# Kernel optimization log

Hardware: AMD Instinct MI355X
Metric: run time of the kernel (lower is better)

The kernel has to match this reference:

```python
import jax, jax.numpy as jnp
import numpy as np

B, C, H, W = 16, 64, 64, 64
HEADS = 8

def conv1x1(x, w):
    # x: [B, Cin, H, W], w: [Cout, Cin] -> [B, Cout, H, W]
    return jnp.einsum('oc,bchw->bohw', w, x)

def maxpool2x2(x):
    b, c, h, w = x.shape
    return x.reshape(b, c, h // 2, 2, w // 2, 2).max(axis=(3, 5))

def setup_inputs() -> dict:
    key = jax.random.key(0)
    ks = jax.random.split(key, 6)
    x = jax.random.normal(ks[0], (B, C, H, W), dtype=jnp.float32)
    w_theta = jax.random.normal(ks[1], (C // HEADS, C), dtype=jnp.float32) * 0.05
    w_phi = jax.random.normal(ks[2], (C // HEADS, C), dtype=jnp.float32) * 0.05
    w_g = jax.random.normal(ks[3], (C // 2, C), dtype=jnp.float32) * 0.05
    w_o = jax.random.normal(ks[4], (C, C // 2), dtype=jnp.float32) * 0.05
    gamma = jax.random.normal(ks[5], (), dtype=jnp.float32)
    return {'x': x, 'w_theta': w_theta, 'w_phi': w_phi, 'w_g': w_g, 'w_o': w_o, 'gamma': gamma}

def reference(x, w_theta, w_phi, w_g, w_o, gamma):
    b, c, h, w = x.shape
    n = h * w                      # query length
    m = n // 4                     # kv length after 2x2 maxpool
    theta = conv1x1(x, w_theta).reshape(b, c // HEADS, n)   # [B, C/h, N]
    phi = maxpool2x2(conv1x1(x, w_phi)).reshape(b, c // HEADS, m)  # [B, C/h, M]
    g = maxpool2x2(conv1x1(x, w_g)).reshape(b, c // 2, m)   # [B, C/2, M]
    # attention: theta^T @ phi -> [B, N, M]; NOTE: no 1/sqrt(d) scaling (SAGAN)
    beta = jax.nn.softmax(jnp.einsum('bdn,bdm->bnm', theta, phi), axis=-1)
    # o = g @ beta^T -> [B, C/2, N]
    o = jnp.einsum('bdm,bnm->bdn', g, beta).reshape(b, c // 2, h, w)
    o = conv1x1(o, w_o)            # [B, C, H, W]
    return gamma * o + x
```

## Files before the change

kernel.cpp:

```cpp
#include <hip/hip_runtime.h>
#include <hip/hip_bf16.h>

#define NB 16
#define NC 64
#define NN 4096
#define NM 1024
#define ND 8
#define NG 32

typedef short short8 __attribute__((ext_vector_type(8)));
typedef float floatx4 __attribute__((ext_vector_type(4)));

#define LOG2E 1.44269504f

__device__ __forceinline__ short f2bfs(float f) {
    union { __hip_bfloat16 h; short s; } u;
    u.h = __float2bfloat16(f);
    return u.s;
}
__device__ __forceinline__ unsigned pack2bf(float a, float b) {
    return (unsigned)(unsigned short)f2bfs(a) | ((unsigned)(unsigned short)f2bfs(b) << 16);
}
__device__ __forceinline__ unsigned pk2fast(float a, float b) {
    unsigned ua = __float_as_uint(a) + 0x8000u;
    unsigned ub = __float_as_uint(b) + 0x8000u;
    return __builtin_amdgcn_perm(ub, ua, 0x07060302);
}
__device__ __forceinline__ short8 u4s8(uint4 v) {
    union { uint4 u; short8 s; } c; c.u = v; return c.s;
}

__global__ __launch_bounds__(256)
void proj_kernel(const float* __restrict__ x,
                 const float* __restrict__ w_theta,
                 const float* __restrict__ w_phi,
                 const float* __restrict__ w_g,
                 const float* __restrict__ w_o,
                 unsigned* __restrict__ theta_ws,
                 unsigned* __restrict__ phi_ws,
                 unsigned* __restrict__ g2_ws)
{
    __shared__ __align__(16) float xl[64 * 128];
    __shared__ float lwt[512];
    __shared__ float lwp[512];
    __shared__ __align__(8) float lwgT[64 * 34];
    __shared__ float lwoT[32 * 65];
    __shared__ __align__(16) float lgs[32 * 36];
    __shared__ float lps[32 * 8];

    const int b  = blockIdx.x >> 5;
    const int ph = blockIdx.x & 31;
    const int t  = threadIdx.x;

    for (int i = t; i < 512;  i += 256) { lwt[i] = w_theta[i]; lwp[i] = w_phi[i]; }
    for (int i = t; i < 2048; i += 256) {
        lwgT[(i & 63) * 34 + (i >> 6)] = w_g[i];
        lwoT[(i & 31) * 65 + (i >> 5)] = w_o[i];
    }

    const float* xb = x + (size_t)b * NC * NN + (size_t)ph * 128;
    for (int idx = t; idx < 2048; idx += 256) {
        int c = idx >> 5, i4 = idx & 31;
        ((float4*)xl)[c * 32 + i4] = ((const float4*)(xb + (size_t)c * NN))[i4];
    }
    __syncthreads();

    if (t < 128) {
        float th[8];
        #pragma unroll
        for (int oc = 0; oc < 8; ++oc) th[oc] = 0.f;
        for (int c = 0; c < 64; ++c) {
            float xv = xl[c * 128 + t];
            #pragma unroll
            for (int oc = 0; oc < 8; ++oc) th[oc] = fmaf(lwt[oc * 64 + c], xv, th[oc]);
        }
        uint4 pk;
        pk.x = pack2bf(th[0] * LOG2E, th[1] * LOG2E);
        pk.y = pack2bf(th[2] * LOG2E, th[3] * LOG2E);
        pk.z = pack2bf(th[4] * LOG2E, th[5] * LOG2E);
        pk.w = pack2bf(th[6] * LOG2E, th[7] * LOG2E);
        ((uint4*)theta_ws)[(size_t)b * NN + ph * 128 + t] = pk;

        int m = t >> 2, oc0 = (t & 3) * 2;
        float s[2][4];
        #pragma unroll
        for (int a = 0; a < 2; ++a)
            #pragma unroll
            for (int p = 0; p < 4; ++p) s[a][p] = 0.f;
        #pragma unroll 4
        for (int c = 0; c < 64; ++c) {
            const float* xr = &xl[c * 128];
            float x0 = xr[2 * m], x1 = xr[2 * m + 1], x2 = xr[64 + 2 * m], x3 = xr[65 + 2 * m];
            #pragma unroll
            for (int a = 0; a < 2; ++a) {
                float w = lwp[(oc0 + a) * 64 + c];
                s[a][0] = fmaf(w, x0, s[a][0]);
                s[a][1] = fmaf(w, x1, s[a][1]);
                s[a][2] = fmaf(w, x2, s[a][2]);
                s[a][3] = fmaf(w, x3, s[a][3]);
            }
        }
        #pragma unroll
        for (int a = 0; a < 2; ++a)
            lps[m * 8 + oc0 + a] = fmaxf(fmaxf(s[a][0], s[a][1]), fmaxf(s[a][2], s[a][3]));
    } else {
        int tt = t - 128;
        int oc0 = (tt >> 3) * 2, grp = tt & 7;
        float s0[16], s1[16];
        #pragma unroll
        for (int i = 0; i < 16; ++i) { s0[i] = 0.f; s1[i] = 0.f; }
        const float4* xl4 = (const float4*)xl;
        #pragma unroll 2
        for (int c = 0; c < 64; ++c) {
            float4 a0 = xl4[c * 32 + 2 * grp];
            float4 a1 = xl4[c * 32 + 2 * grp + 1];
            float4 b0 = xl4[c * 32 + 16 + 2 * grp];
            float4 b1 = xl4[c * 32 + 17 + 2 * grp];
            float2 wv = *(const float2*)&lwgT[c * 34 + oc0];
            float w0 = wv.x, w1 = wv.y;
            s0[0] = fmaf(w0, a0.x, s0[0]);  s0[1] = fmaf(w0, a0.y, s0[1]);
            s0[2] = fmaf(w0, a0.z, s0[2]);  s0[3] = fmaf(w0, a0.w, s0[3]);
            s0[4] = fmaf(w0, a1.x, s0[4]);  s0[5] = fmaf(w0, a1.y, s0[5]);
            s0[6] = fmaf(w0, a1.z, s0[6]);  s0[7] = fmaf(w0, a1.w, s0[7]);
            s0[8] = fmaf(w0, b0.x, s0[8]);  s0[9] = fmaf(w0, b0.y, s0[9]);
            s0[10] = fmaf(w0, b0.z, s0[10]); s0[11] = fmaf(w0, b0.w, s0[11]);
            s0[12] = fmaf(w0, b1.x, s0[12]); s0[13] = fmaf(w0, b1.y, s0[13]);
            s0[14] = fmaf(w0, b1.z, s0[14]); s0[15] = fmaf(w0, b1.w, s0[15]);
            s1[0] = fmaf(w1, a0.x, s1[0]);  s1[1] = fmaf(w1, a0.y, s1[1]);
            s1[2] = fmaf(w1, a0.z, s1[2]);  s1[3] = fmaf(w1, a0.w, s1[3]);
            s1[4] = fmaf(w1, a1.x, s1[4]);  s1[5] = fmaf(w1, a1.y, s1[5]);
            s1[6] = fmaf(w1, a1.z, s1[6]);  s1[7] = fmaf(w1, a1.w, s1[7]);
            s1[8] = fmaf(w1, b0.x, s1[8]);  s1[9] = fmaf(w1, b0.y, s1[9]);
            s1[10] = fmaf(w1, b0.z, s1[10]); s1[11] = fmaf(w1, b0.w, s1[11]);
            s1[12] = fmaf(w1, b1.x, s1[12]); s1[13] = fmaf(w1, b1.y, s1[13]);
            s1[14] = fmaf(w1, b1.z, s1[14]); s1[15] = fmaf(w1, b1.w, s1[15]);
        }
        #pragma unroll
        for (int p = 0; p < 4; ++p) {
            float v0 = fmaxf(fmaxf(s0[2 * p], s0[2 * p + 1]), fmaxf(s0[8 + 2 * p], s0[9 + 2 * p]));
            float v1 = fmaxf(fmaxf(s1[2 * p], s1[2 * p + 1]), fmaxf(s1[8 + 2 * p], s1[9 + 2 * p]));
            lgs[oc0 * 36 + grp * 4 + p]       = v0;
            lgs[(oc0 + 1) * 36 + grp * 4 + p] = v1;
        }
    }
    __syncthreads();

    {
        int co = t >> 2, sel = t & 3;
        int m0a = 4 * sel, m0b = 16 + 4 * sel;
        float v[8];
        #pragma unroll
        for (int mm = 0; mm < 8; ++mm) v[mm] = 0.f;
        #pragma unroll 4
        for (int c = 0; c < 32; ++c) {
            float w = lwoT[c * 65 + co];
            float4 ga = *(const float4*)&lgs[c * 36 + m0a];
            float4 gb = *(const float4*)&lgs[c * 36 + m0b];
            v[0] = fmaf(w, ga.x, v[0]); v[1] = fmaf(w, ga.y, v[1]);
            v[2] = fmaf(w, ga.z, v[2]); v[3] = fmaf(w, ga.w, v[3]);
            v[4] = fmaf(w, gb.x, v[4]); v[5] = fmaf(w, gb.y, v[5]);
            v[6] = fmaf(w, gb.z, v[6]); v[7] = fmaf(w, gb.w, v[7]);
        }
        uint4 pk;
        pk.x = pack2bf(v[0], v[1]); pk.y = pack2bf(v[2], v[3]);
        pk.z = pack2bf(v[4], v[5]); pk.w = pack2bf(v[6], v[7]);
        int lane = (sel << 4) | (co & 15);
        ((uint4*)g2_ws)[(((size_t)b * 4 + (co >> 4)) * 32 + ph) * 64 + lane] = pk;
    }

    if (t < 32) {
        const float* pr = &lps[t * 8];
        uint4 pk;
        pk.x = pack2bf(pr[0], pr[1]); pk.y = pack2bf(pr[2], pr[3]);
        pk.z = pack2bf(pr[4], pr[5]); pk.w = pack2bf(pr[6], pr[7]);
        ((uint4*)phi_ws)[(size_t)b * NM + ph * 32 + t] = pk;
    }
}

#define KG_STEP(CPP0, CPP1, CG)                                                          \
    {                                                                                    \
        _Pragma("unroll")                                                                \
        for (int qt = 0; qt < 2; ++qt) {                                                 \
            floatx4 s0 = __builtin_amdgcn_mfma_f32_16x16x32_bf16(                        \
                u4s8(CPP0), u4s8(tb[qt]), (floatx4)0.f, 0, 0, 0);                        \
            floatx4 s1 = __builtin_amdgcn_mfma_f32_16x16x32_bf16(                        \
                u4s8(CPP1), u4s8(tb[qt]), (floatx4)0.f, 0, 0, 0);                        \
            float e0[4], e1[4];                                                          \
            _Pragma("unroll")                                                            \
            for (int r = 0; r < 4; ++r) {                                                \
                e0[r] = __builtin_amdgcn_exp2f(s0[r]);                                   \
                e1[r] = __builtin_amdgcn_exp2f(s1[r]);                                   \
            }                                                                            \
            lsum[qt] += ((e0[0] + e0[1]) + (e0[2] + e0[3]))                              \
                      + ((e1[0] + e1[1]) + (e1[2] + e1[3]));                             \
            uint4 pq0 = make_uint4(pk2fast(e0[0], e0[1]), pk2fast(e0[2], e0[3]), 0u, 0u);\
            uint4 pq1 = make_uint4(pk2fast(e1[0], e1[1]), pk2fast(e1[2], e1[3]), 0u, 0u);\
            _Pragma("unroll")                                                            \
            for (int ct = 0; ct < 4; ++ct) {                                             \
                acc[qt][ct] = __builtin_amdgcn_mfma_f32_16x16x32_bf16(                   \
                    u4s8(CG[ct]), u4s8(pq0), acc[qt][ct], 0, 0, 0);                      \
                uint4 a1 = make_uint4(CG[ct].z, CG[ct].w, CG[ct].z, CG[ct].w);           \
                acc[qt][ct] = __builtin_amdgcn_mfma_f32_16x16x32_bf16(                   \
                    u4s8(a1), u4s8(pq1), acc[qt][ct], 0, 0, 0);                          \
            }                                                                            \
        }                                                                                \
    }

__global__ __launch_bounds__(256, 2)
void attn_kernel(const unsigned* __restrict__ theta_ws,
                 const unsigned* __restrict__ phi_ws,
                 const unsigned* __restrict__ g2_ws,
                 const float* __restrict__ gamma_p,
                 const float* __restrict__ x,
                 float* __restrict__ out)
{
    __shared__ __align__(16) float smem_f[64 * 140];
    uint4* lphi = (uint4*)smem_f;
    float* ltr  = smem_f;

    const int b    = blockIdx.x >> 5;
    const int qblk = blockIdx.x & 31;
    const int t    = threadIdx.x;
    const int w    = t >> 6;
    const int lane = t & 63;
    const int lm   = lane & 15;
    const int quad = lane >> 4;
    const int q0   = qblk * 128 + w * 32;

    for (int kk = t; kk < NM; kk += 256)
        lphi[kk] = ((const uint4*)phi_ws)[(size_t)b * NM + kk];

    uint4 tb[2];
    #pragma unroll
    for (int qt = 0; qt < 2; ++qt) {
        uint4 v = ((const uint4*)theta_ws)[(size_t)b * NN + q0 + qt * 16 + lm];
        tb[qt].x = quad == 0 ? v.x : 0u;
        tb[qt].y = quad == 0 ? v.y : 0u;
        tb[qt].z = quad == 0 ? v.z : 0u;
        tb[qt].w = quad == 0 ? v.w : 0u;
    }

    floatx4 acc[2][4];
    #pragma unroll
    for (int qt = 0; qt < 2; ++qt)
        #pragma unroll
        for (int ct = 0; ct < 4; ++ct) acc[qt][ct] = (floatx4)0.f;
    float lsum[2] = {0.f, 0.f};

    const uint4* gf = (const uint4*)g2_ws;
    uint4 gA[4], gB[4];
    #pragma unroll
    for (int ct = 0; ct < 4; ++ct) {
        gA[ct] = gf[(((size_t)b * 4 + ct) * 32 + 0) * 64 + lane];
        gB[ct] = gf[(((size_t)b * 4 + ct) * 32 + 1) * 64 + lane];
    }

    __syncthreads();

    uint4 qA0 = lphi[lm],      qA1 = lphi[16 + lm];
    uint4 qB0 = lphi[32 + lm], qB1 = lphi[48 + lm];

    for (int kg2 = 0; kg2 < 16; ++kg2) {
        {
            uint4 c0 = qA0, c1 = qA1;
            uint4 cg[4] = {gA[0], gA[1], gA[2], gA[3]};
            if (kg2 < 15) {
                int nk = 2 * kg2 + 2;
                qA0 = lphi[nk * 32 + lm];
                qA1 = lphi[nk * 32 + 16 + lm];
                #pragma unroll
                for (int ct = 0; ct < 4; ++ct)
                    gA[ct] = gf[(((size_t)b * 4 + ct) * 32 + nk) * 64 + lane];
            }
            KG_STEP(c0, c1, cg);
        }
        {
            uint4 c0 = qB0, c1 = qB1;
            uint4 cg[4] = {gB[0], gB[1], gB[2], gB[3]};
            if (kg2 < 15) {
                int nk = 2 * kg2 + 3;
                qB0 = lphi[nk * 32 + lm];
                qB1 = lphi[nk * 32 + 16 + lm];
                #pragma unroll
                for (int ct = 0; ct < 4; ++ct)
                    gB[ct] = gf[(((size_t)b * 4 + ct) * 32 + nk) * 64 + lane];
            }
            KG_STEP(c0, c1, cg);
        }
    }

    float inv[2];
    {
        float l0 = lsum[0]; l0 += __shfl_xor(l0, 16); l0 += __shfl_xor(l0, 32);
        float l1 = lsum[1]; l1 += __shfl_xor(l1, 16); l1 += __shfl_xor(l1, 32);
        inv[0] = 1.0f / l0; inv[1] = 1.0f / l1;
    }

    const float gamma = gamma_p[0];

    __syncthreads();
    #pragma unroll
    for (int qt = 0; qt < 2; ++qt)
        #pragma unroll
        for (int ct = 0; ct < 4; ++ct)
            #pragma unroll
            for (int r = 0; r < 4; ++r)
                ltr[(ct * 16 + quad * 4 + r) * 140 + w * 32 + qt * 16 + lm]
                    = acc[qt][ct][r] * inv[qt];
    __syncthreads();

    {
        const int l16 = t & 15;
        #pragma unroll
        for (int io = 0; io < 4; ++io) {
            int co = io * 16 + (t >> 4);
            size_t base = ((size_t)b * NC + co) * NN + qblk * 128 + l16 * 8;
            const float* tr = &ltr[co * 140 + l16 * 8];
            float4 t0 = ((const float4*)tr)[0];
            float4 t1 = ((const float4*)tr)[1];
            float4 x0 = *(const float4*)(x + base);
            float4 x1 = *(const float4*)(x + base + 4);
            float4 o0 = make_float4(fmaf(gamma, t0.x, x0.x), fmaf(gamma, t0.y, x0.y),
                                    fmaf(gamma, t0.z, x0.z), fmaf(gamma, t0.w, x0.w));
            float4 o1 = make_float4(fmaf(gamma, t1.x, x1.x), fmaf(gamma, t1.y, x1.y),
                                    fmaf(gamma, t1.z, x1.z), fmaf(gamma, t1.w, x1.w));
            *(float4*)(out + base)     = o0;
            *(float4*)(out + base + 4) = o1;
        }
    }
}

extern "C" void kernel_launch(void* const* d_in, const int* in_sizes, int n_in,
                              void* d_out, int out_size, void* d_ws, size_t ws_size,
                              hipStream_t stream)
{
    const float* x  = (const float*)d_in[0];
    const float* wt = (const float*)d_in[1];
    const float* wp = (const float*)d_in[2];
    const float* wg = (const float*)d_in[3];
    const float* wo = (const float*)d_in[4];
    const float* gm = (const float*)d_in[5];
    float* out = (float*)d_out;

    unsigned* theta_ws = (unsigned*)d_ws;
    unsigned* phi_ws   = theta_ws + (size_t)NB * NN * ND / 2;
    unsigned* g2_ws    = phi_ws   + (size_t)NB * NM * ND / 2;

    proj_kernel<<<NB * 32, 256, 0, stream>>>(x, wt, wp, wg, wo, theta_ws, phi_ws, g2_ws);
    attn_kernel<<<NB * 32, 256, 0, stream>>>(theta_ws, phi_ws, g2_ws, gm, x, out);
}
```

Measured before the change: 113.3 us.

## Fuse theta projection into attention kernel and halve PV MFMA count

Theta is no longer computed in the projection kernel and round-tripped through workspace. The attention kernel now loads its own x tile and w_theta into shared memory and computes theta locally before the main loop. The projection kernel's thread split is rebalanced so every thread does one g channel and one phi output. The PV step packs both exponential halves into one bf16 operand, issuing one MFMA per channel tile instead of two. This adds an extra x read and two barriers in the attention kernel, plus more shared memory, which may reduce occupancy.

```diff
diff --git a/kernel.cpp b/kernel.cpp
--- a/kernel.cpp
+++ b/kernel.cpp
@@ -32,17 +32,14 @@
 
 __global__ __launch_bounds__(256)
 void proj_kernel(const float* __restrict__ x,
-                 const float* __restrict__ w_theta,
                  const float* __restrict__ w_phi,
                  const float* __restrict__ w_g,
                  const float* __restrict__ w_o,
-                 unsigned* __restrict__ theta_ws,
                  unsigned* __restrict__ phi_ws,
                  unsigned* __restrict__ g2_ws)
 {
     __shared__ __align__(16) float xl[64 * 128];
-    __shared__ float lwt[512];
-    __shared__ float lwp[512];
+    __shared__ float lwpT[64 * 8];
     __shared__ __align__(8) float lwgT[64 * 34];
     __shared__ float lwoT[32 * 65];
     __shared__ __align__(16) float lgs[32 * 36];
@@ -52,7 +49,7 @@
     const int ph = blockIdx.x & 31;
     const int t  = threadIdx.x;
 
-    for (int i = t; i < 512;  i += 256) { lwt[i] = w_theta[i]; lwp[i] = w_phi[i]; }
+    for (int i = t; i < 512; i += 256) lwpT[(i & 63) * 8 + (i >> 6)] = w_phi[i];
     for (int i = t; i < 2048; i += 256) {
         lwgT[(i & 63) * 34 + (i >> 6)] = w_g[i];
         lwoT[(i & 31) * 65 + (i >> 5)] = w_o[i];
@@ -65,59 +62,19 @@
     }
     __syncthreads();
 
-    if (t < 128) {
-        float th[8];
-        #pragma unroll
-        for (int oc = 0; oc < 8; ++oc) th[oc] = 0.f;
-        for (int c = 0; c < 64; ++c) {
-            float xv = xl[c * 128 + t];
-            #pragma unroll
-            for (int oc = 0; oc < 8; ++oc) th[oc] = fmaf(lwt[oc * 64 + c], xv, th[oc]);
-        }
-        uint4 pk;
-        pk.x = pack2bf(th[0] * LOG2E, th[1] * LOG2E);
-        pk.y = pack2bf(th[2] * LOG2E, th[3] * LOG2E);
-        pk.z = pack2bf(th[4] * LOG2E, th[5] * LOG2E);
-        pk.w = pack2bf(th[6] * LOG2E, th[7] * LOG2E);
-        ((uint4*)theta_ws)[(size_t)b * NN + ph * 128 + t] = pk;
-
-        int m = t >> 2, oc0 = (t & 3) * 2;
-        float s[2][4];
-        #pragma unroll
-        for (int a = 0; a < 2; ++a)
-            #pragma unroll
-            for (int p = 0; p < 4; ++p) s[a][p] = 0.f;
+    {
+        int oc = t >> 3, grp = t & 7;
+        float s0[16];
+        #pragma unroll
+        for (int i = 0; i < 16; ++i) s0[i] = 0.f;
+        const float4* xl4 = (const float4*)xl;
         #pragma unroll 4
-        for (int c = 0; c < 64; ++c) {
-            const float* xr = &xl[c * 128];
-            float x0 = xr[2 * m], x1 = xr[2 * m + 1], x2 = xr[64 + 2 * m], x3 = xr[65 + 2 * m];
-            #pragma unroll
-            for (int a = 0; a < 2; ++a) {
-                float w = lwp[(oc0 + a) * 64 + c];
-                s[a][0] = fmaf(w, x0, s[a][0]);
-                s[a][1] = fmaf(w, x1, s[a][1]);
-                s[a][2] = fmaf(w, x2, s[a][2]);
-                s[a][3] = fmaf(w, x3, s[a][3]);
-            }
-        }
-        #pragma unroll
-        for (int a = 0; a < 2; ++a)
-            lps[m * 8 + oc0 + a] = fmaxf(fmaxf(s[a][0], s[a][1]), fmaxf(s[a][2], s[a][3]));
-    } else {
-        int tt = t - 128;
-        int oc0 = (tt >> 3) * 2, grp = tt & 7;
-        float s0[16], s1[16];
-        #pragma unroll
-        for (int i = 0; i < 16; ++i) { s0[i] = 0.f; s1[i] = 0.f; }
-        const float4* xl4 = (const float4*)xl;
-        #pragma unroll 2
         for (int c = 0; c < 64; ++c) {
             float4 a0 = xl4[c * 32 + 2 * grp];
             float4 a1 = xl4[c * 32 + 2 * grp + 1];
             float4 b0 = xl4[c * 32 + 16 + 2 * grp];
             float4 b1 = xl4[c * 32 + 17 + 2 * grp];
-            float2 wv = *(const float2*)&lwgT[c * 34 + oc0];
-            float w0 = wv.x, w1 = wv.y;
+            float w0 = lwgT[c * 34 + oc];
             s0[0] = fmaf(w0, a0.x, s0[0]);  s0[1] = fmaf(w0, a0.y, s0[1]);
             s0[2] = fmaf(w0, a0.z, s0[2]);  s0[3] = fmaf(w0, a0.w, s0[3]);
             s0[4] = fmaf(w0, a1.x, s0[4]);  s0[5] = fmaf(w0, a1.y, s0[5]);
@@ -126,22 +83,26 @@
             s0[10] = fmaf(w0, b0.z, s0[10]); s0[11] = fmaf(w0, b0.w, s0[11]);
             s0[12] = fmaf(w0, b1.x, s0[12]); s0[13] = fmaf(w0, b1.y, s0[13]);
             s0[14] = fmaf(w0, b1.z, s0[14]); s0[15] = fmaf(w0, b1.w, s0[15]);
-            s1[0] = fmaf(w1, a0.x, s1[0]);  s1[1] = fmaf(w1, a0.y, s1[1]);
-            s1[2] = fmaf(w1, a0.z, s1[2]);  s1[3] = fmaf(w1, a0.w, s1[3]);
-            s1[4] = fmaf(w1, a1.x, s1[4]);  s1[5] = fmaf(w1, a1.y, s1[5]);
-            s1[6] = fmaf(w1, a1.z, s1[6]);  s1[7] = fmaf(w1, a1.w, s1[7]);
-            s1[8] = fmaf(w1, b0.x, s1[8]);  s1[9] = fmaf(w1, b0.y, s1[9]);
-            s1[10] = fmaf(w1, b0.z, s1[10]); s1[11] = fmaf(w1, b0.w, s1[11]);
-            s1[12] = fmaf(w1, b1.x, s1[12]); s1[13] = fmaf(w1, b1.y, s1[13]);
-            s1[14] = fmaf(w1, b1.z, s1[14]); s1[15] = fmaf(w1, b1.w, s1[15]);
-        }
-        #pragma unroll
-        for (int p = 0; p < 4; ++p) {
-            float v0 = fmaxf(fmaxf(s0[2 * p], s0[2 * p + 1]), fmaxf(s0[8 + 2 * p], s0[9 + 2 * p]));
-            float v1 = fmaxf(fmaxf(s1[2 * p], s1[2 * p + 1]), fmaxf(s1[8 + 2 * p], s1[9 + 2 * p]));
-            lgs[oc0 * 36 + grp * 4 + p]       = v0;
-            lgs[(oc0 + 1) * 36 + grp * 4 + p] = v1;
-        }
+        }
+        #pragma unroll
+        for (int p = 0; p < 4; ++p)
+            lgs[oc * 36 + grp * 4 + p] =
+                fmaxf(fmaxf(s0[2 * p], s0[2 * p + 1]), fmaxf(s0[8 + 2 * p], s0[9 + 2 * p]));
+    }
+
+    {
+        int m = t >> 3, oc = t & 7;
+        float s0 = 0.f, s1 = 0.f, s2 = 0.f, s3 = 0.f;
+        #pragma unroll 4
+        for (int c = 0; c < 64; ++c) {
+            float w = lwpT[c * 8 + oc];
+            const float* xr = &xl[c * 128];
+            s0 = fmaf(w, xr[2 * m],      s0);
+            s1 = fmaf(w, xr[2 * m + 1],  s1);
+            s2 = fmaf(w, xr[64 + 2 * m], s2);
+            s3 = fmaf(w, xr[65 + 2 * m], s3);
+        }
+        lps[m * 8 + oc] = fmaxf(fmaxf(s0, s1), fmaxf(s2, s3));
     }
     __syncthreads();
 
@@ -193,30 +154,29 @@
             }                                                                            \
             lsum[qt] += ((e0[0] + e0[1]) + (e0[2] + e0[3]))                              \
                       + ((e1[0] + e1[1]) + (e1[2] + e1[3]));                             \
-            uint4 pq0 = make_uint4(pk2fast(e0[0], e0[1]), pk2fast(e0[2], e0[3]), 0u, 0u);\
-            uint4 pq1 = make_uint4(pk2fast(e1[0], e1[1]), pk2fast(e1[2], e1[3]), 0u, 0u);\
+            uint4 pb = make_uint4(pk2fast(e0[0], e0[1]), pk2fast(e0[2], e0[3]),          \
+                                  pk2fast(e1[0], e1[1]), pk2fast(e1[2], e1[3]));         \
             _Pragma("unroll")                                                            \
-            for (int ct = 0; ct < 4; ++ct) {                                             \
+            for (int ct = 0; ct < 4; ++ct)                                               \
                 acc[qt][ct] = __builtin_amdgcn_mfma_f32_16x16x32_bf16(                   \
-                    u4s8(CG[ct]), u4s8(pq0), acc[qt][ct], 0, 0, 0);                      \
-                uint4 a1 = make_uint4(CG[ct].z, CG[ct].w, CG[ct].z, CG[ct].w);           \
-                acc[qt][ct] = __builtin_amdgcn_mfma_f32_16x16x32_bf16(                   \
-                    u4s8(a1), u4s8(pq1), acc[qt][ct], 0, 0, 0);                          \
-            }                                                                            \
+                    u4s8(CG[ct]), u4s8(pb), acc[qt][ct], 0, 0, 0);                       \
         }                                                                                \
     }
 
 __global__ __launch_bounds__(256, 2)
-void attn_kernel(const unsigned* __restrict__ theta_ws,
-                 const unsigned* __restrict__ phi_ws,
+void attn_kernel(const unsigned* __restrict__ phi_ws,
                  const unsigned* __restrict__ g2_ws,
+                 const float* __restrict__ w_theta,
                  const float* __restrict__ gamma_p,
                  const float* __restrict__ x,
                  float* __restrict__ out)
 {
-    __shared__ __align__(16) float smem_f[64 * 140];
-    uint4* lphi = (uint4*)smem_f;
-    float* ltr  = smem_f;
+    __shared__ __align__(16) float smem[14080];
+    uint4* lphi = (uint4*)smem;
+    float* lwt  = smem + 4096;
+    float* lth  = smem + 4608;
+    float* lx   = smem + 5632;
+    float* ltr  = smem + 4608;
 
     const int b    = blockIdx.x >> 5;
     const int qblk = blockIdx.x & 31;
@@ -227,26 +187,6 @@
     const int quad = lane >> 4;
     const int q0   = qblk * 128 + w * 32;
 
-    for (int kk = t; kk < NM; kk += 256)
-        lphi[kk] = ((const uint4*)phi_ws)[(size_t)b * NM + kk];
-
-    uint4 tb[2];
-    #pragma unroll
-    for (int qt = 0; qt < 2; ++qt) {
-        uint4 v = ((const uint4*)theta_ws)[(size_t)b * NN + q0 + qt * 16 + lm];
-        tb[qt].x = quad == 0 ? v.x : 0u;
-        tb[qt].y = quad == 0 ? v.y : 0u;
-        tb[qt].z = quad == 0 ? v.z : 0u;
-        tb[qt].w = quad == 0 ? v.w : 0u;
-    }
-
-    floatx4 acc[2][4];
-    #pragma unroll
-    for (int qt = 0; qt < 2; ++qt)
-        #pragma unroll
-        for (int ct = 0; ct < 4; ++ct) acc[qt][ct] = (floatx4)0.f;
-    float lsum[2] = {0.f, 0.f};
-
     const uint4* gf = (const uint4*)g2_ws;
     uint4 gA[4], gB[4];
     #pragma unroll
@@ -255,7 +195,53 @@
         gB[ct] = gf[(((size_t)b * 4 + ct) * 32 + 1) * 64 + lane];
     }
 
-    __syncthreads();
+    for (int kk = t; kk < NM; kk += 256)
+        lphi[kk] = ((const uint4*)phi_ws)[(size_t)b * NM + kk];
+    for (int i = t; i < 512; i += 256) lwt[i] = w_theta[i];
+    {
+        const float* xb = x + (size_t)b * NC * NN + (size_t)qblk * 128;
+        for (int idx = t; idx < 2048; idx += 256) {
+            int c = idx >> 5, i4 = idx & 31;
+            ((float4*)(lx + c * 132))[i4] = ((const float4*)(xb + (size_t)c * NN))[i4];
+        }
+    }
+    __syncthreads();
+
+    {
+        int qi = t & 127, och = (t >> 7) * 4;
+        float th4[4] = {0.f, 0.f, 0.f, 0.f};
+        for (int c = 0; c < 64; ++c) {
+            float xv = lx[c * 132 + qi];
+            #pragma unroll
+            for (int o = 0; o < 4; ++o)
+                th4[o] = fmaf(lwt[(och + o) * 64 + c], xv, th4[o]);
+        }
+        *(float4*)&lth[qi * 8 + och] = make_float4(th4[0], th4[1], th4[2], th4[3]);
+    }
+    __syncthreads();
+
+    uint4 tb[2];
+    #pragma unroll
+    for (int qt = 0; qt < 2; ++qt) {
+        const float* thp = &lth[(w * 32 + qt * 16 + lm) * 8];
+        float4 a = ((const float4*)thp)[0], c4 = ((const float4*)thp)[1];
+        uint4 v;
+        v.x = pack2bf(a.x * LOG2E, a.y * LOG2E);
+        v.y = pack2bf(a.z * LOG2E, a.w * LOG2E);
+        v.z = pack2bf(c4.x * LOG2E, c4.y * LOG2E);
+        v.w = pack2bf(c4.z * LOG2E, c4.w * LOG2E);
+        tb[qt].x = quad == 0 ? v.x : 0u;
+        tb[qt].y = quad == 0 ? v.y : 0u;
+        tb[qt].z = quad == 0 ? v.z : 0u;
+        tb[qt].w = quad == 0 ? v.w : 0u;
+    }
+
+    floatx4 acc[2][4];
+    #pragma unroll
+    for (int qt = 0; qt < 2; ++qt)
+        #pragma unroll
+        for (int ct = 0; ct < 4; ++ct) acc[qt][ct] = (floatx4)0.f;
+    float lsum[2] = {0.f, 0.f};
 
     uint4 qA0 = lphi[lm],      qA1 = lphi[16 + lm];
     uint4 qB0 = lphi[32 + lm], qB1 = lphi[48 + lm];
@@ -342,10 +328,9 @@
     const float* gm = (const float*)d_in[5];
     float* out = (float*)d_out;
 
-    unsigned* theta_ws = (unsigned*)d_ws;
-    unsigned* phi_ws   = theta_ws + (size_t)NB * NN * ND / 2;
-    unsigned* g2_ws    = phi_ws   + (size_t)NB * NM * ND / 2;
-
-    proj_kernel<<<NB * 32, 256, 0, stream>>>(x, wt, wp, wg, wo, theta_ws, phi_ws, g2_ws);
-    attn_kernel<<<NB * 32, 256, 0, stream>>>(theta_ws, phi_ws, g2_ws, gm, x, out);
-}
+    unsigned* phi_ws = (unsigned*)d_ws;
+    unsigned* g2_ws  = phi_ws + (size_t)NB * NM * ND / 2;
+
+    proj_kernel<<<NB * 32, 256, 0, stream>>>(x, wp, wg, wo, phi_ws, g2_ws);
+    attn_kernel<<<NB * 32, 256, 0, stream>>>(phi_ws, g2_ws, wt, gm, x, out);
+}
```

Measured after the change: 113.2 us. No clear change (-0.1%).
